# Kernel tuning notes

Measured on AMD Instinct MI355X. Metric: run time of the kernel, lower is better.

## Reference

```python
import jax, jax.numpy as jnp
import numpy as np

N_NODES = 50000
N_EDGES = 800000
HIDDEN = 128
BN_EPS = 1e-5


def setup_inputs() -> dict:
    key = jax.random.key(0)
    ks = jax.random.split(key, 4)
    x = jax.random.normal(ks[0], (N_NODES, HIDDEN), dtype=jnp.float32)
    edge_index = jax.random.randint(ks[1], (2, N_EDGES), 0, N_NODES, dtype=jnp.int64)
    scale = 1.0 / np.sqrt(HIDDEN)
    W1 = jax.random.normal(ks[2], (HIDDEN, HIDDEN), dtype=jnp.float32) * scale
    b1 = jnp.zeros((HIDDEN,), dtype=jnp.float32)
    W2 = jax.random.normal(ks[3], (HIDDEN, HIDDEN), dtype=jnp.float32) * scale
    b2 = jnp.zeros((HIDDEN,), dtype=jnp.float32)
    gamma = jnp.ones((HIDDEN,), dtype=jnp.float32)
    beta = jnp.zeros((HIDDEN,), dtype=jnp.float32)
    return {"x": x, "edge_index": edge_index, "W1": W1, "b1": b1,
            "W2": W2, "b2": b2, "gamma": gamma, "beta": beta}


def reference(x, edge_index, W1, b1, W2, b2, gamma, beta):
    # GINConv (eps=0): h_i = MLP( x_i + sum_{(j->i) in E} x_j )
    src = edge_index[0]
    dst = edge_index[1]
    agg = jax.ops.segment_sum(x[src], dst, num_segments=x.shape[0])  # [N, H]
    h = x + agg
    # 2-layer MLP: Linear -> ReLU -> Linear
    h = jnp.maximum(h @ W1 + b1, 0.0)
    h = h @ W2 + b2
    # BatchNorm1d over node dimension (training-mode batch statistics)
    mean = jnp.mean(h, axis=0)
    var = jnp.var(h, axis=0)
    h = (h - mean) * jax.lax.rsqrt(var + BN_EPS) * gamma + beta
    # add_activation=False (default): no ReLU. Dropout in eval mode: identity.
    return h
```

## Files before the change

kernel.cpp:

```cpp
#include <hip/hip_runtime.h>

typedef unsigned int u32;
typedef unsigned short u16;
typedef __attribute__((ext_vector_type(8))) short short8;
typedef __attribute__((ext_vector_type(4))) float f32x4;

static constexpr int NN = 50000;
static constexpr int NE = 800000;
static constexpr int HH = 128;
static constexpr int NB1 = (NN + 1023) / 1024;
static constexpr int NBK = 196;
static constexpr int EPB = 8192;
static constexpr int NEB = (NE + EPB - 1) / EPB;

__device__ __forceinline__ u32 bf16r(float f) {
  u32 u = __builtin_bit_cast(u32, f);
  return (u + 0x7FFFu + ((u >> 16) & 1u)) >> 16;
}
__device__ __forceinline__ u32 pk2(float lo, float hi) { return bf16r(lo) | (bf16r(hi) << 16); }
__device__ __forceinline__ float bl(u32 p) { return __builtin_bit_cast(float, p << 16); }
__device__ __forceinline__ float bh(u32 p) { return __builtin_bit_cast(float, p & 0xFFFF0000u); }

__global__ __launch_bounds__(256) void prep_kernel(const float4* __restrict__ x,
                                                   uint4* __restrict__ x16,
                                                   const float* __restrict__ W1,
                                                   u16* __restrict__ w1t,
                                                   const float* __restrict__ W2,
                                                   u16* __restrict__ w2t,
                                                   float* __restrict__ stats,
                                                   const int* __restrict__ ei,
                                                   int* __restrict__ hist2d) {
  __shared__ int hist[NBK];
  const int b = blockIdx.x, t = threadIdx.x;
  if (b < 3125) {
    const int i = b * 256 + t;
    const float4 a = x[2 * i];
    const float4 c = x[2 * i + 1];
    uint4 o;
    o.x = pk2(a.x, a.y);
    o.y = pk2(a.z, a.w);
    o.z = pk2(c.x, c.y);
    o.w = pk2(c.z, c.w);
    x16[i] = o;
  } else if (b < 3189) {
    const int o = (b - 3125) * 256 + t;
    const int n = o >> 7, k = o & 127;
    w1t[o] = (u16)bf16r(W1[k * 128 + n]);
  } else if (b < 3253) {
    const int o = (b - 3189) * 256 + t;
    const int n = o >> 7, k = o & 127;
    w2t[o] = (u16)bf16r(W2[k * 128 + n]);
  } else if (b == 3253) {
    stats[t] = 0.f;
  } else {
    const int hb = b - 3254;
    for (int i = t; i < NBK; i += 256) hist[i] = 0;
    __syncthreads();
    const int e0 = hb * EPB;
    const int e1 = min(e0 + EPB, NE);
    for (int e = e0 + t; e < e1; e += 256) atomicAdd(&hist[ei[NE + e] >> 8], 1);
    __syncthreads();
    for (int i = t; i < NBK; i += 256) hist2d[hb * NBK + i] = hist[i];
  }
}

__global__ __launch_bounds__(256) void ph2_kernel(const int* __restrict__ hist2d,
                                                  int* __restrict__ block_base,
                                                  int* __restrict__ bucket_offs,
                                                  int* __restrict__ offs) {
  __shared__ int tsum[256];
  const int t = threadIdx.x;
  int total = 0;
  if (t < NBK)
    for (int b = 0; b < NEB; ++b) total += hist2d[b * NBK + t];
  tsum[t] = total;
  __syncthreads();
  for (int off = 1; off < 256; off <<= 1) {
    const int add = (t >= off) ? tsum[t - off] : 0;
    __syncthreads();
    tsum[t] += add;
    __syncthreads();
  }
  const int excl = t ? tsum[t - 1] : 0;
  if (t < NBK) {
    bucket_offs[t] = excl;
    int run = excl;
    for (int b = 0; b < NEB; ++b) {
      block_base[b * NBK + t] = run;
      run += hist2d[b * NBK + t];
    }
  }
  if (t == 0) {
    bucket_offs[NBK] = NE;
    offs[NN] = NE;
  }
}

__global__ __launch_bounds__(256) void ph3_kernel(const int* __restrict__ ei,
                                                  const int* __restrict__ block_base,
                                                  u32* __restrict__ packed) {
  __shared__ int cur[NBK];
  const int b = blockIdx.x, t = threadIdx.x;
  for (int i = t; i < NBK; i += 256) cur[i] = block_base[b * NBK + i];
  __syncthreads();
  const int e0 = b * EPB;
  const int e1 = min(e0 + EPB, NE);
  for (int e = e0 + t; e < e1; e += 256) {
    const int s = ei[e];
    const int d = ei[NE + e];
    const int pos = atomicAdd(&cur[d >> 8], 1);
    packed[pos] = (u32)s | ((u32)(d & 255) << 16);
  }
}

__global__ __launch_bounds__(256) void ph4_kernel(const u32* __restrict__ packed,
                                                  const int* __restrict__ bucket_offs,
                                                  int* __restrict__ offs,
                                                  int* __restrict__ srcl) {
  __shared__ int hist[256];
  __shared__ int scn[256];
  const int b = blockIdx.x, t = threadIdx.x;
  const int base = bucket_offs[b];
  const int cnt = bucket_offs[b + 1] - base;
  hist[t] = 0;
  __syncthreads();
  for (int i = t; i < cnt; i += 256) atomicAdd(&hist[packed[base + i] >> 16], 1);
  __syncthreads();
  scn[t] = hist[t];
  __syncthreads();
  for (int off = 1; off < 256; off <<= 1) {
    const int add = (t >= off) ? scn[t - off] : 0;
    __syncthreads();
    scn[t] += add;
    __syncthreads();
  }
  const int excl = t ? scn[t - 1] : 0;
  const int node = b * 256 + t;
  if (node < NN) offs[node] = base + excl;
  __syncthreads();
  hist[t] = excl;
  __syncthreads();
  for (int i = t; i < cnt; i += 256) {
    const u32 p = packed[base + i];
    const int r = atomicAdd(&hist[p >> 16], 1);
    srcl[base + r] = (int)(p & 0xFFFFu);
  }
}

__global__ __launch_bounds__(256) void gather16_kernel(const u32* __restrict__ x16,
                                                       const int* __restrict__ offs,
                                                       const int* __restrict__ srcl,
                                                       u32* __restrict__ h0) {
  const int hw = (blockIdx.x * 256 + threadIdx.x) >> 5;
  const int l31 = threadIdx.x & 31;
  const int nhw = gridDim.x * 8;
  for (int node = hw; node < NN; node += nhw) {
    const uint2 sv = reinterpret_cast<const uint2*>(x16 + (size_t)node * 64)[l31];
    float a0 = bl(sv.x), a1 = bh(sv.x), a2 = bl(sv.y), a3 = bh(sv.y);
    const int beg = offs[node], end = offs[node + 1];
    int e = beg;
    for (; e + 8 <= end; e += 8) {
      int s[8];
#pragma unroll
      for (int j = 0; j < 8; ++j) s[j] = srcl[e + j];
      uint2 v[8];
#pragma unroll
      for (int j = 0; j < 8; ++j)
        v[j] = reinterpret_cast<const uint2*>(x16 + (size_t)s[j] * 64)[l31];
#pragma unroll
      for (int j = 0; j < 8; ++j) {
        a0 += bl(v[j].x); a1 += bh(v[j].x);
        a2 += bl(v[j].y); a3 += bh(v[j].y);
      }
    }
    for (; e < end; ++e) {
      const uint2 v = reinterpret_cast<const uint2*>(x16 + (size_t)srcl[e] * 64)[l31];
      a0 += bl(v.x); a1 += bh(v.x);
      a2 += bl(v.y); a3 += bh(v.y);
    }
    uint2 o;
    o.x = pk2(a0, a1);
    o.y = pk2(a2, a3);
    reinterpret_cast<uint2*>(h0 + (size_t)node * 64)[l31] = o;
  }
}

__global__ __launch_bounds__(256) void fused_mlp_kernel(const u16* __restrict__ h0,
                                                        const u16* __restrict__ w1t,
                                                        const float* __restrict__ b1,
                                                        const u16* __restrict__ w2t,
                                                        const float* __restrict__ b2,
                                                        u32* __restrict__ h2,
                                                        float* __restrict__ stats,
                                                        int nchunk) {
  __shared__ __align__(16) u16 hs[16][136];
  __shared__ float sstats[256];
  const int t = threadIdx.x;
  const int w = t >> 6;
  const int lane = t & 63;
  const int lhi = lane >> 4, llo = lane & 15;
  sstats[t] = 0.f;

  short8 w1f[2][4], w2f[2][4];
  float4 bs1[2], bs2[2];
#pragma unroll
  for (int c = 0; c < 2; ++c) {
    const int ct = 2 * w + c;
#pragma unroll
    for (int kb = 0; kb < 4; ++kb) {
      w1f[c][kb] = *reinterpret_cast<const short8*>(w1t + (size_t)(16 * ct + llo) * 128 + kb * 32 + lhi * 8);
      w2f[c][kb] = *reinterpret_cast<const short8*>(w2t + (size_t)(16 * ct + llo) * 128 + kb * 32 + lhi * 8);
    }
    bs1[c] = *reinterpret_cast<const float4*>(b1 + ct * 16 + lhi * 4);
    bs2[c] = *reinterpret_cast<const float4*>(b2 + ct * 16 + lhi * 4);
  }
  __syncthreads();

  for (int ch = blockIdx.x; ch < nchunk; ch += gridDim.x) {
    const int row0 = ch * 16;

    const u16* arow = h0 + (size_t)(row0 + llo) * 128;
    short8 afr[4];
#pragma unroll
    for (int kb = 0; kb < 4; ++kb)
      afr[kb] = *reinterpret_cast<const short8*>(arow + kb * 32 + lhi * 8);

    f32x4 acc0 = {0.f, 0.f, 0.f, 0.f};
    f32x4 acc1 = {0.f, 0.f, 0.f, 0.f};
#pragma unroll
    for (int kb = 0; kb < 4; ++kb) {
      acc0 = __builtin_amdgcn_mfma_f32_16x16x32_bf16(w1f[0][kb], afr[kb], acc0, 0, 0, 0);
      acc1 = __builtin_amdgcn_mfma_f32_16x16x32_bf16(w1f[1][kb], afr[kb], acc1, 0, 0, 0);
    }

#pragma unroll
    for (int c = 0; c < 2; ++c) {
      const int ct = 2 * w + c;
      const f32x4 a = c ? acc1 : acc0;
      const float4 bb = c ? bs1[1] : bs1[0];
      const float v0 = fmaxf(a[0] + bb.x, 0.f);
      const float v1 = fmaxf(a[1] + bb.y, 0.f);
      const float v2 = fmaxf(a[2] + bb.z, 0.f);
      const float v3 = fmaxf(a[3] + bb.w, 0.f);
      u32* dst = reinterpret_cast<u32*>(&hs[llo][ct * 16 + lhi * 4]);
      dst[0] = pk2(v0, v1);
      dst[1] = pk2(v2, v3);
    }
    __syncthreads();

    short8 af2[4];
#pragma unroll
    for (int kb = 0; kb < 4; ++kb)
      af2[kb] = *reinterpret_cast<const short8*>(&hs[llo][kb * 32 + lhi * 8]);

    f32x4 dcc0 = {0.f, 0.f, 0.f, 0.f};
    f32x4 dcc1 = {0.f, 0.f, 0.f, 0.f};
#pragma unroll
    for (int kb = 0; kb < 4; ++kb) {
      dcc0 = __builtin_amdgcn_mfma_f32_16x16x32_bf16(w2f[0][kb], af2[kb], dcc0, 0, 0, 0);
      dcc1 = __builtin_amdgcn_mfma_f32_16x16x32_bf16(w2f[1][kb], af2[kb], dcc1, 0, 0, 0);
    }
    __syncthreads();

#pragma unroll
    for (int c = 0; c < 2; ++c) {
      const int ct = 2 * w + c;
      const f32x4 a = c ? dcc1 : dcc0;
      const float4 bb = c ? bs2[1] : bs2[0];
      float v0 = a[0] + bb.x;
      float v1 = a[1] + bb.y;
      float v2 = a[2] + bb.z;
      float v3 = a[3] + bb.w;
      u32* op = h2 + (size_t)(row0 + llo) * 64 + ct * 8 + lhi * 2;
      op[0] = pk2(v0, v1);
      op[1] = pk2(v2, v3);
      float q0 = v0 * v0, q1 = v1 * v1, q2 = v2 * v2, q3 = v3 * v3;
#pragma unroll
      for (int m = 1; m < 16; m <<= 1) {
        v0 += __shfl_xor(v0, m, 64); v1 += __shfl_xor(v1, m, 64);
        v2 += __shfl_xor(v2, m, 64); v3 += __shfl_xor(v3, m, 64);
        q0 += __shfl_xor(q0, m, 64); q1 += __shfl_xor(q1, m, 64);
        q2 += __shfl_xor(q2, m, 64); q3 += __shfl_xor(q3, m, 64);
      }
      if (llo == 0) {
        const int cb = ct * 16 + lhi * 4;
        atomicAdd(&sstats[cb + 0], v0); atomicAdd(&sstats[cb + 1], v1);
        atomicAdd(&sstats[cb + 2], v2); atomicAdd(&sstats[cb + 3], v3);
        atomicAdd(&sstats[128 + cb + 0], q0); atomicAdd(&sstats[128 + cb + 1], q1);
        atomicAdd(&sstats[128 + cb + 2], q2); atomicAdd(&sstats[128 + cb + 3], q3);
      }
    }
  }
  __syncthreads();
  atomicAdd(&stats[t], sstats[t]);
}

__global__ __launch_bounds__(256) void bn16_kernel(const u32* __restrict__ h2,
                                                   const float* __restrict__ stats,
                                                   const float* __restrict__ gamma,
                                                   const float* __restrict__ beta,
                                                   float* __restrict__ out, float invn) {
  __shared__ float scale_s[128], shift_s[128];
  const int t = threadIdx.x;
  if (t < 128) {
    const float mean = stats[t] * invn;
    float var = fmaf(-mean, mean, stats[128 + t] * invn);
    var = fmaxf(var, 0.f);
    const float rs = rsqrtf(var + 1e-5f);
    const float sc = gamma[t] * rs;
    scale_s[t] = sc;
    shift_s[t] = fmaf(-mean, sc, beta[t]);
  }
  __syncthreads();
  int i = blockIdx.x * 256 + t;
  const int stride = gridDim.x * 256;
  for (; i < NN * 64; i += stride) {
    const int c = (i & 63) * 2;
    const u32 p = h2[i];
    float2 o;
    o.x = fmaf(bl(p), scale_s[c + 0], shift_s[c + 0]);
    o.y = fmaf(bh(p), scale_s[c + 1], shift_s[c + 1]);
    *reinterpret_cast<float2*>(out + 2 * (size_t)i) = o;
  }
}

__global__ void zero_stats_kernel(float* __restrict__ stats) { stats[threadIdx.x] = 0.f; }

__global__ __launch_bounds__(256) void zero_int_kernel(int* __restrict__ p, int n) {
  int i = blockIdx.x * blockDim.x + threadIdx.x;
  const int stride = gridDim.x * blockDim.x;
  for (; i < n; i += stride) p[i] = 0;
}

__global__ __launch_bounds__(256) void count_kernel(const int* __restrict__ ei,
                                                    int* __restrict__ cnt) {
  const int e = blockIdx.x * blockDim.x + threadIdx.x;
  if (e < NE) atomicAdd(&cnt[ei[NE + e]], 1);
}

__global__ __launch_bounds__(256) void scan1_kernel(const int* __restrict__ cnt,
                                                    int* __restrict__ offs,
                                                    int* __restrict__ partials) {
  __shared__ int tsum[256];
  const int b = blockIdx.x, t = threadIdx.x;
  const int base = b * 1024 + t * 4;
  int v[4];
  int s = 0;
#pragma unroll
  for (int j = 0; j < 4; ++j) {
    const int idx = base + j;
    v[j] = (idx < NN) ? cnt[idx] : 0;
    s += v[j];
  }
  tsum[t] = s;
  __syncthreads();
#pragma unroll
  for (int off = 1; off < 256; off <<= 1) {
    const int add = (t >= off) ? tsum[t - off] : 0;
    __syncthreads();
    tsum[t] += add;
    __syncthreads();
  }
  int excl = (t ? tsum[t - 1] : 0);
#pragma unroll
  for (int j = 0; j < 4; ++j) {
    const int idx = base + j;
    if (idx < NN) offs[idx] = excl;
    excl += v[j];
  }
  if (t == 255) partials[b] = tsum[255];
}

__global__ void scan2_kernel(int* __restrict__ partials, int nb) {
  const int t = threadIdx.x;
  int v = (t < nb) ? partials[t] : 0;
#pragma unroll
  for (int off = 1; off < 64; off <<= 1) {
    const int n = __shfl_up(v, off, 64);
    if (t >= off) v += n;
  }
  int excl = __shfl_up(v, 1, 64);
  if (t == 0) excl = 0;
  if (t < nb) partials[t] = excl;
}

__global__ __launch_bounds__(256) void scan3_kernel(int* __restrict__ offs,
                                                    int* __restrict__ cursor,
                                                    const int* __restrict__ partials) {
  const int b = blockIdx.x;
  const int add = partials[b];
#pragma unroll
  for (int j = 0; j < 4; ++j) {
    const int idx = b * 1024 + threadIdx.x + j * 256;
    if (idx < NN) {
      const int o = offs[idx] + add;
      offs[idx] = o;
      cursor[idx] = o;
    }
  }
  if (b == 0 && threadIdx.x == 0) offs[NN] = NE;
}

__global__ __launch_bounds__(256) void fill_kernel(const int* __restrict__ ei,
                                                   int* __restrict__ cursor,
                                                   int* __restrict__ srcl) {
  const int e = blockIdx.x * blockDim.x + threadIdx.x;
  if (e >= NE) return;
  const int s = ei[e];
  const int d = ei[NE + e];
  const int pos = atomicAdd(&cursor[d], 1);
  srcl[pos] = s;
}

__global__ __launch_bounds__(256) void gather_kernel(const float* __restrict__ x,
                                                     const int* __restrict__ offs,
                                                     const int* __restrict__ srcl,
                                                     float* __restrict__ out) {
  const int wave = (blockIdx.x * 256 + threadIdx.x) >> 6;
  const int lane = threadIdx.x & 63;
  const int nwaves = gridDim.x * 4;
  for (int node = wave; node < NN; node += nwaves) {
    float2 acc = *reinterpret_cast<const float2*>(x + (size_t)node * HH + lane * 2);
    const int beg = offs[node], end = offs[node + 1];
    for (int e = beg; e < end; ++e) {
      const int s = srcl[e];
      const float2 v = *reinterpret_cast<const float2*>(x + (size_t)s * HH + lane * 2);
      acc.x += v.x;
      acc.y += v.y;
    }
    *reinterpret_cast<float2*>(out + (size_t)node * HH + lane * 2) = acc;
  }
}

__global__ __launch_bounds__(256) void copy_x_kernel(const float4* __restrict__ x,
                                                     float4* __restrict__ h, int n4) {
  int i = blockIdx.x * blockDim.x + threadIdx.x;
  const int stride = gridDim.x * blockDim.x;
  for (; i < n4; i += stride) h[i] = x[i];
}

__global__ __launch_bounds__(256) void scatter_kernel(const float* __restrict__ x,
                                                      const int* __restrict__ ei,
                                                      float* __restrict__ h) {
  const long long tid = (long long)blockIdx.x * blockDim.x + threadIdx.x;
  const int e = (int)(tid >> 5);
  if (e >= NE) return;
  const int c = (int)(tid & 31);
  const int s = ei[e];
  const int d = ei[NE + e];
  const float4 v = *reinterpret_cast<const float4*>(x + (size_t)s * HH + c * 4);
  float* dp = h + (size_t)d * HH + c * 4;
  atomicAdd(dp + 0, v.x);
  atomicAdd(dp + 1, v.y);
  atomicAdd(dp + 2, v.z);
  atomicAdd(dp + 3, v.w);
}

template <bool RELU>
__global__ __launch_bounds__(256, 2) void gemm128_kernel(const float* in,
                                                         const float* __restrict__ W,
                                                         const float* __restrict__ bias,
                                                         float* out,
                                                         int nrows, int nchunks) {
  __shared__ float Ws[128][128];
  __shared__ float rows_s[32][128];
  const int t = threadIdx.x;
  for (int i = t; i < 128 * 128 / 4; i += 256) {
    reinterpret_cast<float4*>(&Ws[0][0])[i] = reinterpret_cast<const float4*>(W)[i];
  }
  const int col4 = (t & 31) * 4;
  const int rowg = (t >> 5) * 4;
  const float4 b4 = *reinterpret_cast<const float4*>(bias + col4);

  for (int chunk = blockIdx.x; chunk < nchunks; chunk += gridDim.x) {
    const int row0 = chunk * 32;
    __syncthreads();
    for (int i = t; i < 1024; i += 256) {
      const int rr = i >> 5, cc = (i & 31) * 4;
      const int grow = row0 + rr;
      float4 v = make_float4(0.f, 0.f, 0.f, 0.f);
      if (grow < nrows) v = *reinterpret_cast<const float4*>(in + (size_t)grow * HH + cc);
      *reinterpret_cast<float4*>(&rows_s[rr][cc]) = v;
    }
    __syncthreads();

    float acc[4][4] = {};
#pragma unroll 4
    for (int k = 0; k < 128; k += 4) {
      float4 a[4];
#pragma unroll
      for (int r = 0; r < 4; ++r) a[r] = *reinterpret_cast<const float4*>(&rows_s[rowg + r][k]);
#pragma unroll
      for (int kk = 0; kk < 4; ++kk) {
        const float4 wv = *reinterpret_cast<const float4*>(&Ws[k + kk][col4]);
#pragma unroll
        for (int r = 0; r < 4; ++r) {
          const float av = (&a[r].x)[kk];
          acc[r][0] = fmaf(av, wv.x, acc[r][0]);
          acc[r][1] = fmaf(av, wv.y, acc[r][1]);
          acc[r][2] = fmaf(av, wv.z, acc[r][2]);
          acc[r][3] = fmaf(av, wv.w, acc[r][3]);
        }
      }
    }

#pragma unroll
    for (int r = 0; r < 4; ++r) {
      const int grow = row0 + rowg + r;
      if (grow < nrows) {
        float4 o;
        o.x = acc[r][0] + b4.x;
        o.y = acc[r][1] + b4.y;
        o.z = acc[r][2] + b4.z;
        o.w = acc[r][3] + b4.w;
        if (RELU) {
          o.x = fmaxf(o.x, 0.f); o.y = fmaxf(o.y, 0.f);
          o.z = fmaxf(o.z, 0.f); o.w = fmaxf(o.w, 0.f);
        }
        *reinterpret_cast<float4*>(out + (size_t)grow * HH + col4) = o;
      }
    }
  }
}

__global__ __launch_bounds__(256) void col_stats_kernel(const float* __restrict__ h,
                                                        float* __restrict__ stats, int nrows) {
  __shared__ float ssum[256], ssq[256];
  const int t = threadIdx.x;
  const int col = t & 127;
  const int half = t >> 7;
  float s = 0.f, q = 0.f;
  for (int r = blockIdx.x * 2 + half; r < nrows; r += gridDim.x * 2) {
    const float v = h[(size_t)r * HH + col];
    s += v;
    q = fmaf(v, v, q);
  }
  ssum[t] = s;
  ssq[t] = q;
  __syncthreads();
  if (t < 128) {
    atomicAdd(&stats[col], ssum[t] + ssum[t + 128]);
    atomicAdd(&stats[128 + col], ssq[t] + ssq[t + 128]);
  }
}

__global__ __launch_bounds__(256) void bn_apply_kernel(float* __restrict__ h,
                                                       const float* __restrict__ stats,
                                                       const float* __restrict__ gamma,
                                                       const float* __restrict__ beta,
                                                       int n4, float invn) {
  __shared__ float scale_s[128], shift_s[128];
  const int t = threadIdx.x;
  if (t < 128) {
    const float mean = stats[t] * invn;
    float var = fmaf(-mean, mean, stats[128 + t] * invn);
    var = fmaxf(var, 0.f);
    const float rs = rsqrtf(var + 1e-5f);
    const float sc = gamma[t] * rs;
    scale_s[t] = sc;
    shift_s[t] = fmaf(-mean, sc, beta[t]);
  }
  __syncthreads();
  float4* h4 = reinterpret_cast<float4*>(h);
  int i = blockIdx.x * blockDim.x + threadIdx.x;
  const int stride = gridDim.x * blockDim.x;
  for (; i < n4; i += stride) {
    const int c = (i & 31) * 4;
    float4 v = h4[i];
    v.x = fmaf(v.x, scale_s[c + 0], shift_s[c + 0]);
    v.y = fmaf(v.y, scale_s[c + 1], shift_s[c + 1]);
    v.z = fmaf(v.z, scale_s[c + 2], shift_s[c + 2]);
    v.w = fmaf(v.w, scale_s[c + 3], shift_s[c + 3]);
    h4[i] = v;
  }
}

extern "C" void kernel_launch(void* const* d_in, const int* in_sizes, int n_in,
                              void* d_out, int out_size, void* d_ws, size_t ws_size,
                              hipStream_t stream) {
  const float* x = (const float*)d_in[0];
  const int* ei = (const int*)d_in[1];
  const float* W1 = (const float*)d_in[2];
  const float* b1 = (const float*)d_in[3];
  const float* W2 = (const float*)d_in[4];
  const float* b2 = (const float*)d_in[5];
  const float* gamma = (const float*)d_in[6];
  const float* beta = (const float*)d_in[7];
  float* out = (float*)d_out;

  auto AL = [](size_t v) { return (v + 255) & ~(size_t)255; };
  const size_t offs_b = AL((size_t)(NN + 1) * 4);
  const size_t srcl_b = AL((size_t)NE * 4);
  const size_t packed_b = AL((size_t)NE * 4);
  const size_t h2d_b = AL((size_t)NEB * NBK * 4);
  const size_t bb_b = AL((size_t)NEB * NBK * 4);
  const size_t boffs_b = AL((size_t)(NBK + 1) * 4);
  const size_t stats_b = AL(256 * 4);
  const size_t x16_b = AL((size_t)NN * HH * 2);
  const size_t wt_b = AL((size_t)128 * 128 * 2);
  const size_t need_A = offs_b + srcl_b + packed_b + h2d_b + bb_b + boffs_b + stats_b +
                        x16_b + 2 * wt_b;

  const size_t cnt_b = AL((size_t)NN * 4);
  const size_t part_b = AL(64 * 4);
  const size_t need_B = offs_b + cnt_b + part_b + srcl_b + stats_b;

  if (ws_size >= need_A) {
    char* p = (char*)d_ws;
    int* offs = (int*)p;       p += offs_b;
    int* srcl = (int*)p;       p += srcl_b;
    u32* packed = (u32*)p;     p += packed_b;
    int* hist2d = (int*)p;     p += h2d_b;
    int* block_base = (int*)p; p += bb_b;
    int* boffs = (int*)p;      p += boffs_b;
    float* stats = (float*)p;  p += stats_b;
    u16* x16 = (u16*)p;        p += x16_b;
    u16* w1t = (u16*)p;        p += wt_b;
    u16* w2t = (u16*)p;

    prep_kernel<<<3254 + NEB, 256, 0, stream>>>((const float4*)x, (uint4*)x16, W1, w1t,
                                                W2, w2t, stats, ei, hist2d);
    ph2_kernel<<<1, 256, 0, stream>>>(hist2d, block_base, boffs, offs);
    ph3_kernel<<<NEB, 256, 0, stream>>>(ei, block_base, packed);
    ph4_kernel<<<NBK, 256, 0, stream>>>(packed, boffs, offs, srcl);

    gather16_kernel<<<2048, 256, 0, stream>>>((const u32*)x16, offs, srcl, (u32*)d_out);

    const int nchunk = NN / 16;
    u32* h2 = (u32*)x16;
    fused_mlp_kernel<<<512, 256, 0, stream>>>((const u16*)d_out, w1t, b1, w2t, b2,
                                              h2, stats, nchunk);
    bn16_kernel<<<2048, 256, 0, stream>>>(h2, stats, gamma, beta, out, 1.0f / NN);
  } else if (ws_size >= need_B) {
    char* p = (char*)d_ws;
    int* offs = (int*)p;      p += offs_b;
    int* cnt = (int*)p;       p += cnt_b;
    int* partials = (int*)p;  p += part_b;
    int* srcl = (int*)p;      p += srcl_b;
    float* stats = (float*)p;

    zero_int_kernel<<<64, 256, 0, stream>>>(cnt, NN);
    count_kernel<<<(NE + 255) / 256, 256, 0, stream>>>(ei, cnt);
    scan1_kernel<<<NB1, 256, 0, stream>>>(cnt, offs, partials);
    scan2_kernel<<<1, 64, 0, stream>>>(partials, NB1);
    scan3_kernel<<<NB1, 256, 0, stream>>>(offs, cnt, partials);
    fill_kernel<<<(NE + 255) / 256, 256, 0, stream>>>(ei, cnt, srcl);
    gather_kernel<<<1024, 256, 0, stream>>>(x, offs, srcl, out);

    zero_stats_kernel<<<1, 256, 0, stream>>>(stats);
    const int nchunks = (NN + 31) / 32;
    gemm128_kernel<true><<<512, 256, 0, stream>>>(out, W1, b1, out, NN, nchunks);
    gemm128_kernel<false><<<512, 256, 0, stream>>>(out, W2, b2, out, NN, nchunks);
    col_stats_kernel<<<1024, 256, 0, stream>>>(out, stats, NN);
    bn_apply_kernel<<<2048, 256, 0, stream>>>(out, stats, gamma, beta, NN * HH / 4, 1.0f / NN);
  } else {
    float* stats = (float*)d_ws;
    copy_x_kernel<<<2048, 256, 0, stream>>>((const float4*)x, (float4*)out, NN * HH / 4);
    const long long sthreads = (long long)NE * 32;
    scatter_kernel<<<(int)((sthreads + 255) / 256), 256, 0, stream>>>(x, ei, out);
    zero_stats_kernel<<<1, 256, 0, stream>>>(stats);
    const int nchunks = (NN + 31) / 32;
    gemm128_kernel<true><<<512, 256, 0, stream>>>(out, W1, b1, out, NN, nchunks);
    gemm128_kernel<false><<<512, 256, 0, stream>>>(out, W2, b2, out, NN, nchunks);
    col_stats_kernel<<<1024, 256, 0, stream>>>(out, stats, NN);
    bn_apply_kernel<<<2048, 256, 0, stream>>>(out, stats, gamma, beta, NN * HH / 4, 1.0f / NN);
  }
}
```

Before: 128.1 us.

## Fuse gather into MLP kernel and fold bucket scan into sort phases

Removes the single-block ph2 scan kernel by having ph3 and ph4 each recompute the bucket totals and prefix sums from hist2d. It also removes the separate gather kernel: each 16-node chunk is aggregated directly into shared memory inside the MLP kernel, so the intermediate h0 round-trip through global memory goes away. The fused kernel runs with a larger grid and uses double shared buffers so one barrier can be dropped. In exchange, every ph3/ph4 block rereads all of hist2d, and gather latency is now serialized with the MFMA work inside each block.

Measured after the change: 145.9 us. 1.14x slower.

```diff
diff --git a/kernel.cpp b/kernel.cpp
--- a/kernel.cpp
+++ b/kernel.cpp
@@ -64,44 +64,29 @@
   }
 }
 
-__global__ __launch_bounds__(256) void ph2_kernel(const int* __restrict__ hist2d,
-                                                  int* __restrict__ block_base,
-                                                  int* __restrict__ bucket_offs,
-                                                  int* __restrict__ offs) {
-  __shared__ int tsum[256];
-  const int t = threadIdx.x;
-  int total = 0;
-  if (t < NBK)
-    for (int b = 0; b < NEB; ++b) total += hist2d[b * NBK + t];
-  tsum[t] = total;
-  __syncthreads();
-  for (int off = 1; off < 256; off <<= 1) {
-    const int add = (t >= off) ? tsum[t - off] : 0;
-    __syncthreads();
-    tsum[t] += add;
-    __syncthreads();
-  }
-  const int excl = t ? tsum[t - 1] : 0;
-  if (t < NBK) {
-    bucket_offs[t] = excl;
-    int run = excl;
-    for (int b = 0; b < NEB; ++b) {
-      block_base[b * NBK + t] = run;
-      run += hist2d[b * NBK + t];
-    }
-  }
-  if (t == 0) {
-    bucket_offs[NBK] = NE;
-    offs[NN] = NE;
-  }
-}
-
 __global__ __launch_bounds__(256) void ph3_kernel(const int* __restrict__ ei,
-                                                  const int* __restrict__ block_base,
+                                                  const int* __restrict__ hist2d,
                                                   u32* __restrict__ packed) {
   __shared__ int cur[NBK];
+  __shared__ int tot[256];
   const int b = blockIdx.x, t = threadIdx.x;
-  for (int i = t; i < NBK; i += 256) cur[i] = block_base[b * NBK + i];
+  int total = 0, partial = 0;
+  if (t < NBK) {
+    for (int bb = 0; bb < NEB; ++bb) {
+      const int v = hist2d[bb * NBK + t];
+      total += v;
+      if (bb < b) partial += v;
+    }
+  }
+  tot[t] = total;
+  __syncthreads();
+  for (int off = 1; off < 256; off <<= 1) {
+    const int add = (t >= off) ? tot[t - off] : 0;
+    __syncthreads();
+    tot[t] += add;
+    __syncthreads();
+  }
+  if (t < NBK) cur[t] = (t ? tot[t - 1] : 0) + partial;
   __syncthreads();
   const int e0 = b * EPB;
   const int e1 = min(e0 + EPB, NE);
@@ -113,15 +98,33 @@
   }
 }
 
-__global__ __launch_bounds__(256) void ph4_kernel(const u32* __restrict__ packed,
-                                                  const int* __restrict__ bucket_offs,
+__global__ __launch_bounds__(256) void ph4_kernel(const int* __restrict__ hist2d,
+                                                  const u32* __restrict__ packed,
                                                   int* __restrict__ offs,
                                                   int* __restrict__ srcl) {
   __shared__ int hist[256];
   __shared__ int scn[256];
+  __shared__ int sb[2];
   const int b = blockIdx.x, t = threadIdx.x;
-  const int base = bucket_offs[b];
-  const int cnt = bucket_offs[b + 1] - base;
+  int total = 0;
+  if (t < NBK)
+    for (int bb = 0; bb < NEB; ++bb) total += hist2d[bb * NBK + t];
+  scn[t] = total;
+  __syncthreads();
+  for (int off = 1; off < 256; off <<= 1) {
+    const int add = (t >= off) ? scn[t - off] : 0;
+    __syncthreads();
+    scn[t] += add;
+    __syncthreads();
+  }
+  if (t == b) {
+    sb[0] = b ? scn[b - 1] : 0;
+    sb[1] = scn[b];
+  }
+  __syncthreads();
+  const int base = sb[0];
+  const int cnt = sb[1] - base;
+
   hist[t] = 0;
   __syncthreads();
   for (int i = t; i < cnt; i += 256) atomicAdd(&hist[packed[base + i] >> 16], 1);
@@ -137,6 +140,7 @@
   const int excl = t ? scn[t - 1] : 0;
   const int node = b * 256 + t;
   if (node < NN) offs[node] = base + excl;
+  if (b == NBK - 1 && t == 0) offs[NN] = NE;
   __syncthreads();
   hist[t] = excl;
   __syncthreads();
@@ -147,58 +151,24 @@
   }
 }
 
-__global__ __launch_bounds__(256) void gather16_kernel(const u32* __restrict__ x16,
-                                                       const int* __restrict__ offs,
-                                                       const int* __restrict__ srcl,
-                                                       u32* __restrict__ h0) {
-  const int hw = (blockIdx.x * 256 + threadIdx.x) >> 5;
-  const int l31 = threadIdx.x & 31;
-  const int nhw = gridDim.x * 8;
-  for (int node = hw; node < NN; node += nhw) {
-    const uint2 sv = reinterpret_cast<const uint2*>(x16 + (size_t)node * 64)[l31];
-    float a0 = bl(sv.x), a1 = bh(sv.x), a2 = bl(sv.y), a3 = bh(sv.y);
-    const int beg = offs[node], end = offs[node + 1];
-    int e = beg;
-    for (; e + 8 <= end; e += 8) {
-      int s[8];
-#pragma unroll
-      for (int j = 0; j < 8; ++j) s[j] = srcl[e + j];
-      uint2 v[8];
-#pragma unroll
-      for (int j = 0; j < 8; ++j)
-        v[j] = reinterpret_cast<const uint2*>(x16 + (size_t)s[j] * 64)[l31];
-#pragma unroll
-      for (int j = 0; j < 8; ++j) {
-        a0 += bl(v[j].x); a1 += bh(v[j].x);
-        a2 += bl(v[j].y); a3 += bh(v[j].y);
-      }
-    }
-    for (; e < end; ++e) {
-      const uint2 v = reinterpret_cast<const uint2*>(x16 + (size_t)srcl[e] * 64)[l31];
-      a0 += bl(v.x); a1 += bh(v.x);
-      a2 += bl(v.y); a3 += bh(v.y);
-    }
-    uint2 o;
-    o.x = pk2(a0, a1);
-    o.y = pk2(a2, a3);
-    reinterpret_cast<uint2*>(h0 + (size_t)node * 64)[l31] = o;
-  }
-}
-
-__global__ __launch_bounds__(256) void fused_mlp_kernel(const u16* __restrict__ h0,
-                                                        const u16* __restrict__ w1t,
-                                                        const float* __restrict__ b1,
-                                                        const u16* __restrict__ w2t,
-                                                        const float* __restrict__ b2,
-                                                        u32* __restrict__ h2,
-                                                        float* __restrict__ stats,
-                                                        int nchunk) {
-  __shared__ __align__(16) u16 hs[16][136];
+__global__ __launch_bounds__(256) void gmlp_kernel(const u32* __restrict__ x16,
+                                                   const int* __restrict__ offs,
+                                                   const int* __restrict__ srcl,
+                                                   const u16* __restrict__ w1t,
+                                                   const float* __restrict__ b1,
+                                                   const u16* __restrict__ w2t,
+                                                   const float* __restrict__ b2,
+                                                   u32* __restrict__ h2,
+                                                   float* __restrict__ stats,
+                                                   int nchunk) {
+  __shared__ __align__(16) u16 hs0[16][136];
+  __shared__ __align__(16) u16 hs1[16][136];
   __shared__ float sstats[256];
   const int t = threadIdx.x;
   const int w = t >> 6;
   const int lane = t & 63;
   const int lhi = lane >> 4, llo = lane & 15;
+  const int q = t >> 4, l16 = t & 15;
   sstats[t] = 0.f;
 
   short8 w1f[2][4], w2f[2][4];
@@ -219,11 +189,49 @@
   for (int ch = blockIdx.x; ch < nchunk; ch += gridDim.x) {
     const int row0 = ch * 16;
 
-    const u16* arow = h0 + (size_t)(row0 + llo) * 128;
+    {
+      const int node = row0 + q;
+      const uint4 sv = reinterpret_cast<const uint4*>(x16 + (size_t)node * 64)[l16];
+      float a0 = bl(sv.x), a1 = bh(sv.x), a2 = bl(sv.y), a3 = bh(sv.y);
+      float a4 = bl(sv.z), a5 = bh(sv.z), a6 = bl(sv.w), a7 = bh(sv.w);
+      const int beg = offs[node], end = offs[node + 1];
+      int e = beg;
+      for (; e + 8 <= end; e += 8) {
+        int s[8];
+#pragma unroll
+        for (int j = 0; j < 8; ++j) s[j] = srcl[e + j];
+        uint4 v[8];
+#pragma unroll
+        for (int j = 0; j < 8; ++j)
+          v[j] = reinterpret_cast<const uint4*>(x16 + (size_t)s[j] * 64)[l16];
+#pragma unroll
+        for (int j = 0; j < 8; ++j) {
+          a0 += bl(v[j].x); a1 += bh(v[j].x);
+          a2 += bl(v[j].y); a3 += bh(v[j].y);
+          a4 += bl(v[j].z); a5 += bh(v[j].z);
+          a6 += bl(v[j].w); a7 += bh(v[j].w);
+        }
+      }
+      for (; e < end; ++e) {
+        const uint4 v = reinterpret_cast<const uint4*>(x16 + (size_t)srcl[e] * 64)[l16];
+        a0 += bl(v.x); a1 += bh(v.x);
+        a2 += bl(v.y); a3 += bh(v.y);
+        a4 += bl(v.z); a5 += bh(v.z);
+        a6 += bl(v.w); a7 += bh(v.w);
+      }
+      uint4 o;
+      o.x = pk2(a0, a1);
+      o.y = pk2(a2, a3);
+      o.z = pk2(a4, a5);
+      o.w = pk2(a6, a7);
+      *reinterpret_cast<uint4*>(&hs0[q][l16 * 8]) = o;
+    }
+    __syncthreads();
+
     short8 afr[4];
 #pragma unroll
     for (int kb = 0; kb < 4; ++kb)
-      afr[kb] = *reinterpret_cast<const short8*>(arow + kb * 32 + lhi * 8);
+      afr[kb] = *reinterpret_cast<const short8*>(&hs0[llo][kb * 32 + lhi * 8]);
 
     f32x4 acc0 = {0.f, 0.f, 0.f, 0.f};
     f32x4 acc1 = {0.f, 0.f, 0.f, 0.f};
@@ -242,7 +250,7 @@
       const float v1 = fmaxf(a[1] + bb.y, 0.f);
       const float v2 = fmaxf(a[2] + bb.z, 0.f);
       const float v3 = fmaxf(a[3] + bb.w, 0.f);
-      u32* dst = reinterpret_cast<u32*>(&hs[llo][ct * 16 + lhi * 4]);
+      u32* dst = reinterpret_cast<u32*>(&hs1[llo][ct * 16 + lhi * 4]);
       dst[0] = pk2(v0, v1);
       dst[1] = pk2(v2, v3);
     }
@@ -251,7 +259,7 @@
     short8 af2[4];
 #pragma unroll
     for (int kb = 0; kb < 4; ++kb)
-      af2[kb] = *reinterpret_cast<const short8*>(&hs[llo][kb * 32 + lhi * 8]);
+      af2[kb] = *reinterpret_cast<const short8*>(&hs1[llo][kb * 32 + lhi * 8]);
 
     f32x4 dcc0 = {0.f, 0.f, 0.f, 0.f};
     f32x4 dcc1 = {0.f, 0.f, 0.f, 0.f};
@@ -260,7 +268,6 @@
       dcc0 = __builtin_amdgcn_mfma_f32_16x16x32_bf16(w2f[0][kb], af2[kb], dcc0, 0, 0, 0);
       dcc1 = __builtin_amdgcn_mfma_f32_16x16x32_bf16(w2f[1][kb], af2[kb], dcc1, 0, 0, 0);
     }
-    __syncthreads();
 
 #pragma unroll
     for (int c = 0; c < 2; ++c) {
@@ -593,13 +600,12 @@
   const size_t srcl_b = AL((size_t)NE * 4);
   const size_t packed_b = AL((size_t)NE * 4);
   const size_t h2d_b = AL((size_t)NEB * NBK * 4);
-  const size_t bb_b = AL((size_t)NEB * NBK * 4);
-  const size_t boffs_b = AL((size_t)(NBK + 1) * 4);
   const size_t stats_b = AL(256 * 4);
   const size_t x16_b = AL((size_t)NN * HH * 2);
+  const size_t h2_b = AL((size_t)NN * HH * 2);
   const size_t wt_b = AL((size_t)128 * 128 * 2);
-  const size_t need_A = offs_b + srcl_b + packed_b + h2d_b + bb_b + boffs_b + stats_b +
-                        x16_b + 2 * wt_b;
+  const size_t need_A = offs_b + srcl_b + packed_b + h2d_b + stats_b + x16_b + h2_b +
+                        2 * wt_b;
 
   const size_t cnt_b = AL((size_t)NN * 4);
   const size_t part_b = AL(64 * 4);
@@ -611,25 +617,20 @@
     int* srcl = (int*)p;       p += srcl_b;
     u32* packed = (u32*)p;     p += packed_b;
     int* hist2d = (int*)p;     p += h2d_b;
-    int* block_base = (int*)p; p += bb_b;
-    int* boffs = (int*)p;      p += boffs_b;
     float* stats = (float*)p;  p += stats_b;
     u16* x16 = (u16*)p;        p += x16_b;
+    u32* h2 = (u32*)p;         p += h2_b;
     u16* w1t = (u16*)p;        p += wt_b;
     u16* w2t = (u16*)p;
 
     prep_kernel<<<3254 + NEB, 256, 0, stream>>>((const float4*)x, (uint4*)x16, W1, w1t,
                                                 W2, w2t, stats, ei, hist2d);
-    ph2_kernel<<<1, 256, 0, stream>>>(hist2d, block_base, boffs, offs);
-    ph3_kernel<<<NEB, 256, 0, stream>>>(ei, block_base, packed);
-    ph4_kernel<<<NBK, 256, 0, stream>>>(packed, boffs, offs, srcl);
-
-    gather16_kernel<<<2048, 256, 0, stream>>>((const u32*)x16, offs, srcl, (u32*)d_out);
+    ph3_kernel<<<NEB, 256, 0, stream>>>(ei, hist2d, packed);
+    ph4_kernel<<<NBK, 256, 0, stream>>>(hist2d, packed, offs, srcl);
 
     const int nchunk = NN / 16;
-    u32* h2 = (u32*)x16;
-    fused_mlp_kernel<<<512, 256, 0, stream>>>((const u16*)d_out, w1t, b1, w2t, b2,
-                                              h2, stats, nchunk);
+    gmlp_kernel<<<1024, 256, 0, stream>>>((const u32*)x16, offs, srcl, w1t, b1, w2t, b2,
+                                          h2, stats, nchunk);
     bn16_kernel<<<2048, 256, 0, stream>>>(h2, stats, gamma, beta, out, 1.0f / NN);
   } else if (ws_size >= need_B) {
     char* p = (char*)d_ws;
```
